# Performance work log

Measured on AMD Instinct MI355X. Metric: run time of the kernel, lower is better.

## Reference

```python
import jax, jax.numpy as jnp
import numpy as np
from jax import lax

D_STATE = 16
D_CONV = 4
D_MODEL = 1024
D_INNER = 2048
DT_RANK = 64
SEQLEN = 2048
BATCH = 2


def setup_inputs() -> dict:
    key = jax.random.key(0)
    ks = jax.random.split(key, 8)
    hidden_states = jax.random.normal(ks[0], (SEQLEN, BATCH, D_MODEL), jnp.float32)
    W_in = jax.random.normal(ks[1], (2 * D_INNER, D_MODEL), jnp.float32) * (D_MODEL ** -0.5)
    conv_w = jax.random.normal(ks[2], (D_INNER, D_CONV), jnp.float32) * (D_CONV ** -0.5)
    conv_b = jnp.zeros((D_INNER,), jnp.float32)
    W_x = jax.random.normal(ks[3], (DT_RANK + 2 * D_STATE, D_INNER), jnp.float32) * (D_INNER ** -0.5)
    dt_init_std = DT_RANK ** -0.5
    W_dt = jax.random.uniform(ks[4], (D_INNER, DT_RANK), jnp.float32, -dt_init_std, dt_init_std)
    # dt bias init: inverse-softplus of dt ~ LogUniform(1e-3, 1e-1)
    dt = jnp.exp(jax.random.uniform(ks[5], (D_INNER,), jnp.float32) * (np.log(0.1) - np.log(0.001)) + np.log(0.001))
    dt = jnp.clip(dt, 1e-4, None)
    dt_bias = dt + jnp.log(-jnp.expm1(-dt))
    A_log = jnp.log(jnp.tile(jnp.arange(1, D_STATE + 1, dtype=jnp.float32)[None, :], (D_INNER, 1)))
    Dp = jnp.ones((D_INNER,), jnp.float32)
    W_out = jax.random.normal(ks[6], (D_MODEL, D_INNER), jnp.float32) * (D_INNER ** -0.5)
    return {"hidden_states": hidden_states, "W_in": W_in, "conv_w": conv_w, "conv_b": conv_b,
            "W_x": W_x, "W_dt": W_dt, "dt_bias": dt_bias, "A_log": A_log, "D": Dp, "W_out": W_out}


def _mamba_forward(hidden_states, W_in, conv_w, conv_b, W_x, W_dt, dt_bias, A_log, D, W_out):
    L, B, _ = hidden_states.shape
    d_inner, d_state = A_log.shape
    dt_rank = W_dt.shape[1]
    # in_proj: [L,B,D] -> [L,B,2*d_inner] -> [B,2*d_inner,L]
    xz = jnp.einsum('lbd,ed->lbe', hidden_states, W_in)
    xz = jnp.transpose(xz, (1, 2, 0))
    x, z = jnp.split(xz, 2, axis=1)  # each [B,d_inner,L]
    # causal depthwise conv1d + silu
    x = lax.conv_general_dilated(x, conv_w[:, None, :], (1,), [(D_CONV - 1, 0)],
                                 dimension_numbers=('NCH', 'OIH', 'NCH'),
                                 feature_group_count=d_inner)
    x = jax.nn.silu(x + conv_b[None, :, None])  # [B,d_inner,L]
    # x_proj over (b l) tokens
    x_bl = jnp.transpose(x, (0, 2, 1)).reshape(B * L, d_inner)  # (b l) d
    x_dbl = x_bl @ W_x.T  # [(b l), dt_rank + 2*d_state]
    dt_lr, Bm, Cm = jnp.split(x_dbl, [dt_rank, dt_rank + d_state], axis=-1)
    dt = (W_dt @ dt_lr.T).reshape(d_inner, B, L).transpose(1, 0, 2)  # [B,d_inner,L]
    Bm = Bm.reshape(B, L, d_state)  # [B,L,n]
    Cm = Cm.reshape(B, L, d_state)
    # selective scan (delta_softplus=True, delta_bias=dt_bias)
    A = -jnp.exp(A_log)  # [d_inner, n]
    delta = jax.nn.softplus(dt + dt_bias[None, :, None])  # [B,d,L]
    delta_t = jnp.transpose(delta, (2, 0, 1))  # [L,B,d]
    u_t = jnp.transpose(x, (2, 0, 1))          # [L,B,d]
    B_t = jnp.transpose(Bm, (1, 0, 2))         # [L,B,n]
    C_t = jnp.transpose(Cm, (1, 0, 2))         # [L,B,n]

    def step(state, inp):
        d_i, u_i, b_i, c_i = inp
        dA = jnp.exp(d_i[:, :, None] * A[None])           # [B,d,n]
        dBu = (d_i * u_i)[:, :, None] * b_i[:, None, :]   # [B,d,n]
        state = state * dA + dBu
        y = jnp.einsum('bdn,bn->bd', state, c_i)
        return state, y

    init = jnp.zeros((B, d_inner, d_state), delta.dtype)
    _, ys = lax.scan(step, init, (delta_t, u_t, B_t, C_t))  # ys [L,B,d]
    y = jnp.transpose(ys, (1, 0, 2))                         # [B,L,d]
    y = y + jnp.transpose(x, (0, 2, 1)) * D[None, None, :]
    y = y * jax.nn.silu(jnp.transpose(z, (0, 2, 1)))
    out = y @ W_out.T  # [B,L,d_model]
    return jnp.transpose(out, (1, 0, 2))  # [L,B,d_model]


def reference(hidden_states, W_in, conv_w, conv_b, W_x, W_dt, dt_bias, A_log, D, W_out):
    return _mamba_forward(hidden_states, W_in, conv_w, conv_b, W_x, W_dt, dt_bias, A_log, D, W_out)
```

## Files before the change

### kernel.cpp

```cpp
#include <hip/hip_runtime.h>
#include <hip/hip_bf16.h>


#define L_SEQ 2048
#define N_B   2
#define D_M   1024
#define D_I   2048
#define D_ST  16
#define R_DT  64
#define CHNK  32
#define CT    64
#define KS    8
#define DUS   68

using bf16 = __hip_bfloat16;
typedef unsigned short u16;
typedef unsigned int u32;
typedef u16 u16x8 __attribute__((ext_vector_type(8)));
typedef __bf16 bf16x8 __attribute__((ext_vector_type(8)));
typedef float f32x4 __attribute__((ext_vector_type(4)));

__device__ __forceinline__ float b2f(u16 u) {
    union { u32 i; float f; } x;
    x.i = ((u32)u) << 16;
    return x.f;
}
__device__ __forceinline__ u16 f2b(float f) {
    union { bf16 h; u16 s; } x;
    x.h = __float2bfloat16(f);
    return x.s;
}

__device__ __forceinline__ void load4(const float* p, float* o) {
    const float4 v = *(const float4*)p;
    o[0] = v.x; o[1] = v.y; o[2] = v.z; o[3] = v.w;
}
__device__ __forceinline__ void load4(const bf16* p, float* o) {
    const ushort4 v = *(const ushort4*)(const void*)p;
    o[0] = b2f(v.x); o[1] = b2f(v.y); o[2] = b2f(v.z); o[3] = b2f(v.w);
}

__device__ __forceinline__ float softplus_f(float x) {
    return (x > 20.f) ? x : log1pf(__expf(x));
}
__device__ __forceinline__ float silu_f(float x) {
    return x / (1.f + __expf(-x));
}

__device__ __forceinline__ void gl_lds16(const u16* g, u16* l) {
    __builtin_amdgcn_global_load_lds(
        (const __attribute__((address_space(1))) void*)g,
        (__attribute__((address_space(3))) void*)l, 16, 0, 0);
}

template <int EPI>
__global__ __launch_bounds__(256) void bgemm(
    const u16* __restrict__ A, int lda,
    const u16* __restrict__ Wb, int ldb, int K,
    u16* __restrict__ bd, float* __restrict__ fout,
    const float* __restrict__ bias)
{
    __shared__ u16 As[128 * 32];
    __shared__ u16 Bs[128 * 32];

    const int tid = threadIdx.x;
    const int m0 = blockIdx.x * 128;
    const int n0 = blockIdx.y * 128;
    const int w  = tid >> 6;
    const int ln = tid & 63;

    const int sr0 = (w << 4) + (ln >> 2);
    const int sr1 = sr0 + 64;
    const int sx  = ln & 3;
    const int qa0 = (sx - (sr0 >> 1)) & 3;
    const int qa1 = (sx - (sr1 >> 1)) & 3;

    const u16* ga0 = A  + (size_t)(m0 + sr0) * lda + qa0 * 8;
    const u16* ga1 = A  + (size_t)(m0 + sr1) * lda + qa1 * 8;
    const u16* gb0 = Wb + (size_t)(n0 + sr0) * ldb + qa0 * 8;
    const u16* gb1 = Wb + (size_t)(n0 + sr1) * ldb + qa1 * 8;
    u16* la0 = As + ((w << 4) + 0) * 32;
    u16* la1 = As + ((w << 4) + 64) * 32;
    u16* lb0 = Bs + ((w << 4) + 0) * 32;
    u16* lb1 = Bs + ((w << 4) + 64) * 32;

    const int wr = (w >> 1) << 6;
    const int wc = (w & 1) << 6;
    const int lm = ln & 15;
    const int qf = ln >> 4;
    int aoff[4], boff[4];
#pragma unroll
    for (int i = 0; i < 4; ++i) {
        const int ra = wr + i * 16 + lm;
        aoff[i] = ra * 32 + (((qf + (ra >> 1)) & 3) << 3);
        const int rb = wc + i * 16 + lm;
        boff[i] = rb * 32 + (((qf + (rb >> 1)) & 3) << 3);
    }

    f32x4 acc[4][4] = {};

    for (int k0 = 0; k0 < K; k0 += 32) {
        if (k0) __syncthreads();
        gl_lds16(ga0 + k0, la0);
        gl_lds16(ga1 + k0, la1);
        gl_lds16(gb0 + k0, lb0);
        gl_lds16(gb1 + k0, lb1);
        __syncthreads();

        bf16x8 af[4], bf[4];
#pragma unroll
        for (int i = 0; i < 4; ++i) af[i] = *(const bf16x8*)&As[aoff[i]];
#pragma unroll
        for (int j = 0; j < 4; ++j) bf[j] = *(const bf16x8*)&Bs[boff[j]];
#pragma unroll
        for (int i = 0; i < 4; ++i)
#pragma unroll
            for (int j = 0; j < 4; ++j)
                acc[i][j] = __builtin_amdgcn_mfma_f32_16x16x32_bf16(
                    af[i], bf[j], acc[i][j], 0, 0, 0);
    }

    const int qr = (ln >> 4) << 2;
    float bv[4];
    if (EPI == 2) {
#pragma unroll
        for (int j = 0; j < 4; ++j) bv[j] = bias[n0 + wc + j * 16 + lm];
    }
#pragma unroll
    for (int i = 0; i < 4; ++i) {
#pragma unroll
        for (int reg = 0; reg < 4; ++reg) {
            const int rg = m0 + wr + i * 16 + qr + reg;
            if (EPI == 0) {
                const int bb = rg & (N_B - 1);
                const int l = rg >> 1;
                const size_t t = (size_t)bb * L_SEQ + l;
#pragma unroll
                for (int j = 0; j < 4; ++j)
                    bd[t * D_I + n0 + wc + j * 16 + lm] = f2b(acc[i][j][reg]);
            } else if (EPI == 1) {
                const int bb = rg >> 11;
                const int l = rg & (L_SEQ - 1);
                const size_t o = ((size_t)l * N_B + bb) * D_M;
#pragma unroll
                for (int j = 0; j < 4; ++j)
                    fout[o + n0 + wc + j * 16 + lm] = acc[i][j][reg];
            } else if (EPI == 2) {
                const size_t t = (size_t)rg;
#pragma unroll
                for (int j = 0; j < 4; ++j)
                    bd[t * D_I + n0 + wc + j * 16 + lm] =
                        f2b(softplus_f(acc[i][j][reg] + bv[j]));
            } else {
                const int bb = rg & (N_B - 1);
                const int l = rg >> 1;
                const size_t t = (size_t)bb * L_SEQ + l;
#pragma unroll
                for (int j = 0; j < 4; ++j) {
                    u16* p = &bd[t * D_I + n0 + wc + j * 16 + lm];
                    *p = f2b(b2f(*p) * silu_f(acc[i][j][reg]));
                }
            }
        }
    }
}

__global__ __launch_bounds__(256) void xproj_k(
    const u16* __restrict__ u, const u16* __restrict__ Wxb,
    float* __restrict__ Part)
{
    __shared__ u16 As[64 * 32];
    __shared__ u16 Bs[96 * 264];

    const int tid = threadIdx.x;
    const int m0 = blockIdx.x * 64;
    const int kc = blockIdx.y;
    const int kbase = kc * 256;

    for (int e = tid; e < 96 * 32; e += 256) {
        const int row = e >> 5, kq = e & 31;
        const u16x8 v = *(const u16x8*)(Wxb + (size_t)row * D_I + kbase + kq * 8);
        *(u16x8*)&Bs[row * 264 + kq * 8] = v;
    }

    const int w  = tid >> 6;
    const int ln = tid & 63;
    const int sr = (w << 4) + (ln >> 2);
    const int sx = ln & 3;
    const int qa = (sx - (sr >> 1)) & 3;
    const u16* ga = u + (size_t)(m0 + sr) * D_I + kbase + qa * 8;
    u16* la = As + (w << 9);

    const int lm = ln & 15;
    const int qf = ln >> 4;
    const int ra = (w << 4) + lm;
    const int aoff = ra * 32 + (((qf + (ra >> 1)) & 3) << 3);

    f32x4 acc[6] = {};

    for (int it = 0; it < 8; ++it) {
        if (it) __syncthreads();
        gl_lds16(ga + it * 32, la);
        __syncthreads();

        const bf16x8 af = *(const bf16x8*)&As[aoff];
#pragma unroll
        for (int j = 0; j < 6; ++j) {
            const bf16x8 bf = *(const bf16x8*)&Bs[(j * 16 + lm) * 264 + it * 32 + qf * 8];
            acc[j] = __builtin_amdgcn_mfma_f32_16x16x32_bf16(af, bf, acc[j], 0, 0, 0);
        }
    }

    const int qr = (ln >> 4) << 2;
#pragma unroll
    for (int j = 0; j < 6; ++j) {
#pragma unroll
        for (int reg = 0; reg < 4; ++reg) {
            const int t = m0 + (w << 4) + qr + reg;
            Part[((size_t)kc * (N_B * L_SEQ) + t) * 96 + j * 16 + lm] = acc[j][reg];
        }
    }
}

__global__ __launch_bounds__(256) void xreduce(
    const float* __restrict__ Part, u16* __restrict__ dtlr,
    float* __restrict__ Bm, float* __restrict__ Cm)
{
    const int e = blockIdx.x * 256 + threadIdx.x;
    const int t = e / 96, c = e - t * 96;
    float s = 0.f;
#pragma unroll
    for (int kc = 0; kc < KS; ++kc)
        s += Part[(size_t)kc * (N_B * L_SEQ * 96) + e];
    if (c < 64)      dtlr[t * 64 + c] = f2b(s);
    else if (c < 80) Bm[t * 16 + (c - 64)] = s;
    else             Cm[t * 16 + (c - 80)] = s;
}

__global__ __launch_bounds__(256) void cvt_k(const float* __restrict__ s,
                                             u16* __restrict__ d)
{
    const size_t i = ((size_t)blockIdx.x * 256 + threadIdx.x) * 8;
    const float4 a = *(const float4*)(s + i);
    const float4 b = *(const float4*)(s + i + 4);
    u16 t[8] = {f2b(a.x), f2b(a.y), f2b(a.z), f2b(a.w),
                f2b(b.x), f2b(b.y), f2b(b.z), f2b(b.w)};
    *(u16x8*)(d + i) = *(const u16x8*)t;
}

__global__ __launch_bounds__(256) void conv_k(
    const bf16* __restrict__ x, const float* __restrict__ cw,
    const float* __restrict__ cb, bf16* __restrict__ xc)
{
    const int t = blockIdx.x;
    const int l = t & (L_SEQ - 1);
#pragma unroll
    for (int it = 0; it < 2; ++it) {
        const int d = ((int)threadIdx.x + it * 256) << 2;
        float w[4][4], bias[4], acc[4];
#pragma unroll
        for (int dd = 0; dd < 4; ++dd)
            load4(cw + (size_t)(d + dd) * 4, w[dd]);
        load4(cb + d, bias);
#pragma unroll
        for (int dd = 0; dd < 4; ++dd) acc[dd] = bias[dd];
#pragma unroll
        for (int j = 0; j < 4; ++j) {
            const int ll = l - 3 + j;
            if (ll >= 0) {
                float xv[4];
                load4(x + (size_t)(t - 3 + j) * D_I + d, xv);
#pragma unroll
                for (int dd = 0; dd < 4; ++dd)
                    acc[dd] = fmaf(xv[dd], w[dd][j], acc[dd]);
            }
        }
        const ushort4 v = make_ushort4(f2b(silu_f(acc[0])), f2b(silu_f(acc[1])),
                                       f2b(silu_f(acc[2])), f2b(silu_f(acc[3])));
        *(ushort4*)(void*)(xc + (size_t)t * D_I + d) = v;
    }
}

template <int PHASE>
__global__ __launch_bounds__(256) void scan_chunk(
    bf16* __restrict__ dy, const bf16* __restrict__ u,
    const float* __restrict__ Bm, const float* __restrict__ Cm,
    const float* __restrict__ Alog, const float* __restrict__ Dp,
    float* __restrict__ Pc, float* __restrict__ Qc,
    const float* __restrict__ Sin)
{
    __shared__ u32 duS[(CT / 2) * DUS];
    __shared__ float Bs[CT][D_ST];
    __shared__ float Cs[(PHASE == 1) ? CT : 1][D_ST];

    const int tid = threadIdx.x;
    const int d0 = blockIdx.x * 64;
    const int b  = blockIdx.y;
    const int c  = blockIdx.z;
    const int row0 = b * L_SEQ + c * CT;

    const int sl = tid >> 3;
    const int sg = tid & 7;

    u32 wB[8];
    {
        const size_t goA = (size_t)(row0 + sl) * D_I + d0 + sg * 8;
        const size_t goB = goA + (size_t)(CT / 2) * D_I;
        const u16x8 dA8 = *(const u16x8*)((const u16*)dy + goA);
        const u16x8 uA8 = *(const u16x8*)((const u16*)u + goA);
        const u16x8 dB8 = *(const u16x8*)((const u16*)dy + goB);
        const u16x8 uB8 = *(const u16x8*)((const u16*)u + goB);
        u32 wA[8];
#pragma unroll
        for (int j = 0; j < 8; ++j) {
            wA[j] = (u32)dA8[j] | ((u32)uA8[j] << 16);
            wB[j] = (u32)dB8[j] | ((u32)uB8[j] << 16);
        }
        *(uint4*)&duS[sl * DUS + sg * 8]     = make_uint4(wA[0], wA[1], wA[2], wA[3]);
        *(uint4*)&duS[sl * DUS + sg * 8 + 4] = make_uint4(wA[4], wA[5], wA[6], wA[7]);
    }
    {
        const float4* src = (const float4*)(Bm + (size_t)row0 * D_ST);
        float4* dst = (float4*)Bs;
        for (int e = tid; e < CT * D_ST / 4; e += 256) dst[e] = src[e];
        if (PHASE == 1) {
            const float4* s2 = (const float4*)(Cm + (size_t)row0 * D_ST);
            float4* d2 = (float4*)Cs;
            for (int e = tid; e < CT * D_ST / 4; e += 256) d2[e] = s2[e];
        }
    }
    __syncthreads();

    const int dl = tid >> 2;
    const int d  = d0 + dl;
    const int ns = tid & 3;
    const size_t pqbase = (((size_t)b * CHNK + c) * D_I + d) * D_ST + ns * 4;

    float Av[4];
    {
        const float4 a4 = *(const float4*)(Alog + (size_t)d * D_ST + ns * 4);
        const float l2e = 1.4426950408889634f;
        Av[0] = -__expf(a4.x) * l2e; Av[1] = -__expf(a4.y) * l2e;
        Av[2] = -__expf(a4.z) * l2e; Av[3] = -__expf(a4.w) * l2e;
    }

    float st[4] = {0.f, 0.f, 0.f, 0.f};
    float sdv = 0.f;
    if (PHASE == 1) {
        const float4 s0 = *(const float4*)(Sin + pqbase);
        st[0] = s0.x; st[1] = s0.y; st[2] = s0.z; st[3] = s0.w;
    }
    const float Dd = (PHASE == 1) ? Dp[d] : 0.f;

#pragma unroll
    for (int half = 0; half < 2; ++half) {
        if (half) {
            __syncthreads();
            if (PHASE == 1) {
                u16 t[8];
#pragma unroll
                for (int j = 0; j < 8; ++j)
                    t[j] = (u16)(duS[sl * DUS + sg * 8 + j] & 0xFFFFu);
                *(u16x8*)((u16*)dy + (size_t)(row0 + sl) * D_I + d0 + sg * 8) =
                    *(const u16x8*)t;
                __syncthreads();
            }
            *(uint4*)&duS[sl * DUS + sg * 8]     = make_uint4(wB[0], wB[1], wB[2], wB[3]);
            *(uint4*)&duS[sl * DUS + sg * 8 + 4] = make_uint4(wB[4], wB[5], wB[6], wB[7]);
            __syncthreads();
        }
        const int lb = half * (CT / 2);
#pragma unroll 2
        for (int l = 0; l < CT / 2; ++l) {
            const u32 w0 = duS[l * DUS + dl];
            union { u32 i; float f; } dvv, uvv;
            dvv.i = w0 << 16;
            uvv.i = w0 & 0xFFFF0000u;
            const float dv = dvv.f, uv = uvv.f;
            const float dvu = dv * uv;

            float bn[4], cn[4] = {0.f, 0.f, 0.f, 0.f};
            {
                const float4 b4 = *(const float4*)&Bs[lb + l][ns * 4];
                bn[0] = b4.x; bn[1] = b4.y; bn[2] = b4.z; bn[3] = b4.w;
            }
            if (PHASE == 1) {
                const float4 c4 = *(const float4*)&Cs[lb + l][ns * 4];
                cn[0] = c4.x; cn[1] = c4.y; cn[2] = c4.z; cn[3] = c4.w;
            }
            if (PHASE == 0) sdv += dv;

            float y = 0.f;
#pragma unroll
            for (int j = 0; j < 4; ++j) {
                const float dA = __builtin_amdgcn_exp2f(dv * Av[j]);
                st[j] = fmaf(st[j], dA, dvu * bn[j]);
                if (PHASE == 1) y = fmaf(st[j], cn[j], y);
            }
            if (PHASE == 1) {
                y += __shfl_xor(y, 1);
                y += __shfl_xor(y, 2);
                if (ns == 0)
                    ((u16*)duS)[(l * DUS + dl) * 2] = f2b(y + uv * Dd);
            }
        }
    }

    if (PHASE == 0) {
        *(float4*)(Pc + pqbase) = make_float4(
            __builtin_amdgcn_exp2f(sdv * Av[0]), __builtin_amdgcn_exp2f(sdv * Av[1]),
            __builtin_amdgcn_exp2f(sdv * Av[2]), __builtin_amdgcn_exp2f(sdv * Av[3]));
        *(float4*)(Qc + pqbase) = make_float4(st[0], st[1], st[2], st[3]);
    } else {
        __syncthreads();
        u16 t[8];
#pragma unroll
        for (int j = 0; j < 8; ++j)
            t[j] = (u16)(duS[sl * DUS + sg * 8 + j] & 0xFFFFu);
        *(u16x8*)((u16*)dy + (size_t)(row0 + CT / 2 + sl) * D_I + d0 + sg * 8) =
            *(const u16x8*)t;
    }
}

__global__ __launch_bounds__(256) void scan_comb(
    const float* Pc, const float* Qc, float* Sin)
{
    const int b = blockIdx.y;
    const int d = blockIdx.x * 16 + (threadIdx.x >> 4);
    const int n = threadIdx.x & 15;
    const size_t i0 = (((size_t)b * CHNK) * D_I + d) * D_ST + n;
    const size_t cs = (size_t)D_I * D_ST;

    float p[CHNK], q[CHNK];
#pragma unroll
    for (int c = 0; c < CHNK; ++c) {
        p[c] = Pc[i0 + c * cs];
        q[c] = Qc[i0 + c * cs];
    }
    float s = 0.f;
#pragma unroll
    for (int c = 0; c < CHNK; ++c) {
        Sin[i0 + c * cs] = s;
        s = fmaf(s, p[c], q[c]);
    }
}

__global__ void zfill(float* o) {
    o[(size_t)blockIdx.x * 256 + threadIdx.x] = 0.f;
}

extern "C" void kernel_launch(void* const* d_in, const int* in_sizes, int n_in,
                              void* d_out, int out_size, void* d_ws, size_t ws_size,
                              hipStream_t stream)
{
    const float* hs   = (const float*)d_in[0];
    const float* Win  = (const float*)d_in[1];
    const float* cw   = (const float*)d_in[2];
    const float* cb   = (const float*)d_in[3];
    const float* Wx   = (const float*)d_in[4];
    const float* Wdt  = (const float*)d_in[5];
    const float* dtb  = (const float*)d_in[6];
    const float* Alog = (const float*)d_in[7];
    const float* Dp   = (const float*)d_in[8];
    const float* Wout = (const float*)d_in[9];
    float* out = (float*)d_out;

    const size_t SZ = (size_t)N_B * L_SEQ * D_I;
    const size_t NT = (size_t)N_B * L_SEQ;
    const size_t NHS   = NT * D_M;
    const size_t NWIN  = (size_t)2 * D_I * D_M;
    const size_t NWOUT = (size_t)D_M * D_I;
    const size_t NWX   = (size_t)96 * D_I;
    const size_t NWDT  = (size_t)D_I * R_DT;
    const size_t NEED = SZ * 2 * sizeof(bf16)
                      + (NHS + NWIN + NWOUT + NWX + NWDT + NT * R_DT) * sizeof(u16)
                      + NT * 2 * D_ST * sizeof(float);
    if (ws_size < NEED) {
        zfill<<<dim3((unsigned)((size_t)out_size / 256)), 256, 0, stream>>>(out);
        return;
    }

    bf16* RA   = (bf16*)d_ws;
    bf16* RB   = RA + SZ;
    u16* bhs   = (u16*)(RB + SZ);
    u16* bWin  = bhs + NHS;
    u16* bWout = bWin + NWIN;
    u16* bWx   = bWout + NWOUT;
    u16* bWdt  = bWx + NWX;
    u16* dtlr  = bWdt + NWDT;
    float* Bm  = (float*)(dtlr + NT * R_DT);
    float* Cm  = Bm + NT * D_ST;
    float* Part = out;
    const size_t PQ = (size_t)N_B * CHNK * D_I * D_ST;
    float* Pc  = out;
    float* Qc  = Pc + PQ;
    float* Sin = Pc;

    cvt_k<<<dim3((unsigned)(NHS / 2048)), 256, 0, stream>>>(hs, bhs);
    cvt_k<<<dim3((unsigned)(NWIN / 2048)), 256, 0, stream>>>(Win, bWin);
    cvt_k<<<dim3((unsigned)(NWOUT / 2048)), 256, 0, stream>>>(Wout, bWout);
    cvt_k<<<dim3((unsigned)(NWX / 2048)), 256, 0, stream>>>(Wx, bWx);
    cvt_k<<<dim3((unsigned)(NWDT / 2048)), 256, 0, stream>>>(Wdt, bWdt);
    bgemm<0><<<dim3(32, 16), 256, 0, stream>>>(
        bhs, D_M, bWin, D_M, D_M, (u16*)RA, nullptr, nullptr);
    conv_k<<<dim3(N_B * L_SEQ), 256, 0, stream>>>(RA, cw, cb, RB);
    xproj_k<<<dim3(64, KS), 256, 0, stream>>>((const u16*)RB, bWx, Part);
    xreduce<<<dim3((unsigned)(NT * 96 / 256)), 256, 0, stream>>>(Part, dtlr, Bm, Cm);
    bgemm<2><<<dim3(32, 16), 256, 0, stream>>>(
        dtlr, R_DT, bWdt, R_DT, R_DT, (u16*)RA, nullptr, dtb);
    scan_chunk<0><<<dim3(D_I / 64, N_B, CHNK), 256, 0, stream>>>(
        RA, RB, Bm, Cm, Alog, Dp, Pc, Qc, nullptr);
    scan_comb<<<dim3(D_I / 16, N_B), 256, 0, stream>>>(Pc, Qc, Sin);
    scan_chunk<1><<<dim3(D_I / 64, N_B, CHNK), 256, 0, stream>>>(
        RA, RB, Bm, Cm, Alog, Dp, nullptr, nullptr, Sin);
    bgemm<3><<<dim3(32, 16), 256, 0, stream>>>(
        bhs, D_M, bWin + (size_t)D_I * D_M, D_M, D_M, (u16*)RA, nullptr, nullptr);
    bgemm<1><<<dim3(32, 8), 256, 0, stream>>>(
        (const u16*)RA, D_I, bWout, D_I, D_I, nullptr, out, nullptr);
}
```

Measured before the change: 348.1 us.

## Triple-buffer LDS tiles in bgemm and xproj with async prefetch two ahead

Both GEMM kernels now keep three LDS stages and issue global-to-LDS loads two k-steps ahead. A single barrier with an explicit vmcnt wait per iteration replaces the two __syncthreads, so global memory latency overlaps the MFMA work. The cost is three times the LDS for the A/B tiles, which may lower occupancy. It also relies on hand-written waitcnt accounting being correct.

```diff
diff --git a/kernel.cpp b/kernel.cpp
--- a/kernel.cpp
+++ b/kernel.cpp
@@ -60,8 +60,8 @@
     u16* __restrict__ bd, float* __restrict__ fout,
     const float* __restrict__ bias)
 {
-    __shared__ u16 As[128 * 32];
-    __shared__ u16 Bs[128 * 32];
+    __shared__ u16 As[3][128 * 32];
+    __shared__ u16 Bs[3][128 * 32];
 
     const int tid = threadIdx.x;
     const int m0 = blockIdx.x * 128;
@@ -79,10 +79,8 @@
     const u16* ga1 = A  + (size_t)(m0 + sr1) * lda + qa1 * 8;
     const u16* gb0 = Wb + (size_t)(n0 + sr0) * ldb + qa0 * 8;
     const u16* gb1 = Wb + (size_t)(n0 + sr1) * ldb + qa1 * 8;
-    u16* la0 = As + ((w << 4) + 0) * 32;
-    u16* la1 = As + ((w << 4) + 64) * 32;
-    u16* lb0 = Bs + ((w << 4) + 0) * 32;
-    u16* lb1 = Bs + ((w << 4) + 64) * 32;
+    const int offL0 = ((w << 4) + 0) * 32;
+    const int offL1 = ((w << 4) + 64) * 32;
 
     const int wr = (w >> 1) << 6;
     const int wc = (w & 1) << 6;
@@ -99,25 +97,51 @@
 
     f32x4 acc[4][4] = {};
 
-    for (int k0 = 0; k0 < K; k0 += 32) {
-        if (k0) __syncthreads();
-        gl_lds16(ga0 + k0, la0);
-        gl_lds16(ga1 + k0, la1);
-        gl_lds16(gb0 + k0, lb0);
-        gl_lds16(gb1 + k0, lb1);
-        __syncthreads();
-
-        bf16x8 af[4], bf[4];
-#pragma unroll
-        for (int i = 0; i < 4; ++i) af[i] = *(const bf16x8*)&As[aoff[i]];
-#pragma unroll
-        for (int j = 0; j < 4; ++j) bf[j] = *(const bf16x8*)&Bs[boff[j]];
+    const int NK = K >> 5;
+    gl_lds16(ga0, As[0] + offL0);
+    gl_lds16(ga1, As[0] + offL1);
+    gl_lds16(gb0, Bs[0] + offL0);
+    gl_lds16(gb1, Bs[0] + offL1);
+    if (NK > 1) {
+        gl_lds16(ga0 + 32, As[1] + offL0);
+        gl_lds16(ga1 + 32, As[1] + offL1);
+        gl_lds16(gb0 + 32, Bs[1] + offL0);
+        gl_lds16(gb1 + 32, Bs[1] + offL1);
+        asm volatile("s_waitcnt vmcnt(4)" ::: "memory");
+    } else {
+        asm volatile("s_waitcnt vmcnt(0)" ::: "memory");
+    }
+    __builtin_amdgcn_s_barrier();
+
+    int cur = 0, nxt = 2;
+    for (int ks = 0; ks < NK; ++ks) {
+        if (ks + 2 < NK) {
+            const int k0 = (ks + 2) << 5;
+            gl_lds16(ga0 + k0, As[nxt] + offL0);
+            gl_lds16(ga1 + k0, As[nxt] + offL1);
+            gl_lds16(gb0 + k0, Bs[nxt] + offL0);
+            gl_lds16(gb1 + k0, Bs[nxt] + offL1);
+        }
+
+        bf16x8 af[4], bfr[4];
+#pragma unroll
+        for (int i = 0; i < 4; ++i) af[i] = *(const bf16x8*)&As[cur][aoff[i]];
+#pragma unroll
+        for (int j = 0; j < 4; ++j) bfr[j] = *(const bf16x8*)&Bs[cur][boff[j]];
 #pragma unroll
         for (int i = 0; i < 4; ++i)
 #pragma unroll
             for (int j = 0; j < 4; ++j)
                 acc[i][j] = __builtin_amdgcn_mfma_f32_16x16x32_bf16(
-                    af[i], bf[j], acc[i][j], 0, 0, 0);
+                    af[i], bfr[j], acc[i][j], 0, 0, 0);
+
+        if (ks + 1 < NK) {
+            if (ks + 2 < NK) asm volatile("s_waitcnt vmcnt(4)" ::: "memory");
+            else             asm volatile("s_waitcnt vmcnt(0)" ::: "memory");
+            __builtin_amdgcn_s_barrier();
+        }
+        cur = (cur == 2) ? 0 : cur + 1;
+        nxt = (nxt == 2) ? 0 : nxt + 1;
     }
 
     const int qr = (ln >> 4) << 2;
@@ -169,7 +193,7 @@
     const u16* __restrict__ u, const u16* __restrict__ Wxb,
     float* __restrict__ Part)
 {
-    __shared__ u16 As[64 * 32];
+    __shared__ u16 As[3][64 * 32];
     __shared__ u16 Bs[96 * 264];
 
     const int tid = threadIdx.x;
@@ -189,7 +213,7 @@
     const int sx = ln & 3;
     const int qa = (sx - (sr >> 1)) & 3;
     const u16* ga = u + (size_t)(m0 + sr) * D_I + kbase + qa * 8;
-    u16* la = As + (w << 9);
+    const int offL = w << 9;
 
     const int lm = ln & 15;
     const int qf = ln >> 4;
@@ -198,16 +222,27 @@
 
     f32x4 acc[6] = {};
 
+    gl_lds16(ga, As[0] + offL);
+    gl_lds16(ga + 32, As[1] + offL);
+    asm volatile("s_waitcnt vmcnt(1) lgkmcnt(0)" ::: "memory");
+    __builtin_amdgcn_s_barrier();
+
+#pragma unroll
     for (int it = 0; it < 8; ++it) {
-        if (it) __syncthreads();
-        gl_lds16(ga + it * 32, la);
-        __syncthreads();
-
-        const bf16x8 af = *(const bf16x8*)&As[aoff];
+        const int cur = it % 3;
+        const int nxt = (it + 2) % 3;
+        if (it + 2 < 8) gl_lds16(ga + (it + 2) * 32, As[nxt] + offL);
+
+        const bf16x8 af = *(const bf16x8*)&As[cur][aoff];
 #pragma unroll
         for (int j = 0; j < 6; ++j) {
-            const bf16x8 bf = *(const bf16x8*)&Bs[(j * 16 + lm) * 264 + it * 32 + qf * 8];
-            acc[j] = __builtin_amdgcn_mfma_f32_16x16x32_bf16(af, bf, acc[j], 0, 0, 0);
+            const bf16x8 bfv = *(const bf16x8*)&Bs[(j * 16 + lm) * 264 + it * 32 + qf * 8];
+            acc[j] = __builtin_amdgcn_mfma_f32_16x16x32_bf16(af, bfv, acc[j], 0, 0, 0);
+        }
+        if (it + 1 < 8) {
+            if (it + 2 < 8) asm volatile("s_waitcnt vmcnt(1)" ::: "memory");
+            else            asm volatile("s_waitcnt vmcnt(0)" ::: "memory");
+            __builtin_amdgcn_s_barrier();
         }
     }
 
```

Result: slower. 356.2 us (+2.3%).
